# Optimization experiments

Hardware: AMD Instinct MI355X
Metric: run time of the kernel (lower is better)

Reference implementation:

```python
import jax, jax.numpy as jnp
import numpy as np

VOCAB, EMBED, HIDDEN, NCLASS = 32000, 256, 512, 2
BATCH, SEQ = 64, 512


def setup_inputs() -> dict:
    key = jax.random.key(0)
    ks = jax.random.split(key, 12)
    s_e = 1.0 / np.sqrt(HIDDEN)  # pytorch RNN init scale
    inp = {
        "x": jax.random.randint(ks[0], (BATCH, SEQ), 0, VOCAB),
        "emb": jax.random.normal(ks[1], (VOCAB, EMBED), dtype=jnp.float32),
        "W_ih0": jax.random.uniform(ks[2], (HIDDEN, EMBED), minval=-s_e, maxval=s_e),
        "W_hh0": jax.random.uniform(ks[3], (HIDDEN, HIDDEN), minval=-s_e, maxval=s_e),
        "b_ih0": jax.random.uniform(ks[4], (HIDDEN,), minval=-s_e, maxval=s_e),
        "b_hh0": jax.random.uniform(ks[5], (HIDDEN,), minval=-s_e, maxval=s_e),
        "W_ih1": jax.random.uniform(ks[6], (HIDDEN, HIDDEN), minval=-s_e, maxval=s_e),
        "W_hh1": jax.random.uniform(ks[7], (HIDDEN, HIDDEN), minval=-s_e, maxval=s_e),
        "b_ih1": jax.random.uniform(ks[8], (HIDDEN,), minval=-s_e, maxval=s_e),
        "b_hh1": jax.random.uniform(ks[9], (HIDDEN,), minval=-s_e, maxval=s_e),
        "W_out": jax.random.uniform(ks[10], (NCLASS, HIDDEN), minval=-s_e, maxval=s_e),
        "b_out": jax.random.uniform(ks[11], (NCLASS,), minval=-s_e, maxval=s_e),
    }
    return inp


def _rnn_layer(inp_bse, W_ih, W_hh, b_ih, b_hh):
    """Vanilla tanh RNN layer. inp: [B,S,E] -> out: [B,S,H]."""
    # precompute input projection for all timesteps (one big GEMM)
    xp = jnp.einsum("bse,he->bsh", inp_bse, W_ih) + b_ih + b_hh  # [B,S,H]
    B = inp_bse.shape[0]
    h0 = jnp.zeros((B, W_hh.shape[0]), dtype=inp_bse.dtype)

    def step(h, xp_t):
        h = jnp.tanh(xp_t + h @ W_hh.T)
        return h, h

    _, out = jax.lax.scan(step, h0, jnp.swapaxes(xp, 0, 1))  # out: [S,B,H]
    return jnp.swapaxes(out, 0, 1)


def reference(x, emb, W_ih0, W_hh0, b_ih0, b_hh0, W_ih1, W_hh1, b_ih1, b_hh1,
              W_out, b_out):
    h = emb[x]  # [B,S,E] embedding lookup
    h = _rnn_layer(h, W_ih0, W_hh0, b_ih0, b_hh0)  # layer 1
    h = _rnn_layer(h, W_ih1, W_hh1, b_ih1, b_hh1)  # layer 2
    pooled = jnp.mean(h, axis=1)  # avg_pool2d over (S,1) == mean over time -> [B,H]
    return pooled @ W_out.T + b_out  # [B,2]
```

## Files before the change

### kernel.cpp

```cpp
#include <hip/hip_runtime.h>
#include <math.h>

#define BB 64
#define SS 512
#define EE 256
#define HH 512

#define NGROUPS 16
#define GSLICES 8
#define LBLK 16
#define BPG 4
#define RECT 512
#define RING 64
#define BARK 32

#define SLOTF (GSLICES * 512)
#define GPKF  (2 * RING * SLOTF)


__global__ void transpose512(const float* __restrict__ in, float* __restrict__ out) {
  __shared__ float tile[32][33];
  int bx = blockIdx.x * 32, by = blockIdx.y * 32;
  int x = threadIdx.x, y0 = threadIdx.y;
  for (int dy = 0; dy < 32; dy += 8)
    tile[y0 + dy][x] = in[(size_t)(by + y0 + dy) * HH + bx + x];
  __syncthreads();
  for (int dy = 0; dy < 32; dy += 8)
    out[(size_t)(bx + y0 + dy) * HH + by + x] = tile[x][y0 + dy];
}

template <int K, bool GATHER>
__global__ __launch_bounds__(256) void xp_gemm(
    const float* __restrict__ Asrc, const int* __restrict__ xidx,
    const float* __restrict__ emb, const float* __restrict__ Wn,
    const float* __restrict__ bias1, const float* __restrict__ bias2,
    float* __restrict__ C) {
  const int tid = threadIdx.x;
  const int m0 = blockIdx.x * 64;
  const int n0 = blockIdx.y * 64;
  __shared__ alignas(16) float As[32][68];
  __shared__ alignas(16) float Bs[32][68];
  __shared__ int xs[64];
  if (GATHER) {
    if (tid < 64) xs[tid] = xidx[m0 + tid];
    __syncthreads();
  }
  float acc[4][4] = {};
  const int ty = tid >> 4, tx = tid & 15;
  const int row = tid >> 2;
  const int kc = (tid & 3) * 8;

  for (int k0 = 0; k0 < K; k0 += 32) {
    const float* ap;
    if (GATHER) ap = emb + (size_t)xs[row] * EE + (k0 + kc);
    else        ap = Asrc + (size_t)(m0 + row) * K + (k0 + kc);
    float4 av0 = *(const float4*)ap;
    float4 av1 = *(const float4*)(ap + 4);
    const float* bp = Wn + (size_t)(n0 + row) * K + (k0 + kc);
    float4 bv0 = *(const float4*)bp;
    float4 bv1 = *(const float4*)(bp + 4);
    __syncthreads();
    As[kc + 0][row] = av0.x; As[kc + 1][row] = av0.y;
    As[kc + 2][row] = av0.z; As[kc + 3][row] = av0.w;
    As[kc + 4][row] = av1.x; As[kc + 5][row] = av1.y;
    As[kc + 6][row] = av1.z; As[kc + 7][row] = av1.w;
    Bs[kc + 0][row] = bv0.x; Bs[kc + 1][row] = bv0.y;
    Bs[kc + 2][row] = bv0.z; Bs[kc + 3][row] = bv0.w;
    Bs[kc + 4][row] = bv1.x; Bs[kc + 5][row] = bv1.y;
    Bs[kc + 6][row] = bv1.z; Bs[kc + 7][row] = bv1.w;
    __syncthreads();
#pragma unroll 8
    for (int k = 0; k < 32; ++k) {
      float4 av = *(const float4*)&As[k][ty * 4];
      float4 bv = *(const float4*)&Bs[k][tx * 4];
      acc[0][0] += av.x * bv.x; acc[0][1] += av.x * bv.y;
      acc[0][2] += av.x * bv.z; acc[0][3] += av.x * bv.w;
      acc[1][0] += av.y * bv.x; acc[1][1] += av.y * bv.y;
      acc[1][2] += av.y * bv.z; acc[1][3] += av.y * bv.w;
      acc[2][0] += av.z * bv.x; acc[2][1] += av.z * bv.y;
      acc[2][2] += av.z * bv.z; acc[2][3] += av.z * bv.w;
      acc[3][0] += av.w * bv.x; acc[3][1] += av.w * bv.y;
      acc[3][2] += av.w * bv.z; acc[3][3] += av.w * bv.w;
    }
  }
  float bj[4];
#pragma unroll
  for (int j = 0; j < 4; ++j) {
    int n = n0 + tx * 4 + j;
    bj[j] = bias1[n] + bias2[n];
  }
#pragma unroll
  for (int i = 0; i < 4; ++i) {
    float4 cv = make_float4(acc[i][0] + bj[0], acc[i][1] + bj[1],
                            acc[i][2] + bj[2], acc[i][3] + bj[3]);
    *(float4*)&C[(size_t)(m0 + ty * 4 + i) * HH + n0 + tx * 4] = cv;
  }
}

__global__ void init_sync(float* __restrict__ pkts, unsigned* __restrict__ flags) {
  const size_t n = (size_t)NGROUPS * GPKF;
  const size_t stride = (size_t)gridDim.x * 256;
  for (size_t i = (size_t)blockIdx.x * 256 + threadIdx.x; i < n; i += stride)
    __hip_atomic_store(&pkts[i], 0.f, __ATOMIC_RELAXED, __HIP_MEMORY_SCOPE_SYSTEM);
  const size_t m = NGROUPS * LBLK * 32;
  for (size_t i = (size_t)blockIdx.x * 256 + threadIdx.x; i < m; i += stride)
    __hip_atomic_store(&flags[i], 0u, __ATOMIC_RELAXED, __HIP_MEMORY_SCOPE_SYSTEM);
}

__device__ __forceinline__ void fma4(float4& d, const float4 w, const float s) {
  d.x = __builtin_fmaf(w.x, s, d.x);
  d.y = __builtin_fmaf(w.y, s, d.y);
  d.z = __builtin_fmaf(w.z, s, d.z);
  d.w = __builtin_fmaf(w.w, s, d.w);
}

__device__ __forceinline__ void poll2(const float* pb, unsigned tg,
                                      float4& u0, float4& u1) {
  for (;;) {
    asm volatile(
      "global_load_dwordx4 %0, %2, off sc0 sc1\n\t"
      "global_load_dwordx4 %1, %2, off offset:16 sc0 sc1\n\t"
      "s_waitcnt vmcnt(0)"
      : "=&v"(u0), "=&v"(u1) : "v"(pb) : "memory");
    if (__float_as_uint(u0.y) == tg && __float_as_uint(u0.w) == tg &&
        __float_as_uint(u1.y) == tg && __float_as_uint(u1.w) == tg) break;
    __builtin_amdgcn_s_sleep(1);
  }
}

__device__ __forceinline__ void poll4(const float* pa, unsigned tga,
                                      const float* pb, unsigned tgb,
                                      float4& a0, float4& a1,
                                      float4& b0, float4& b1) {
  for (;;) {
    asm volatile(
      "global_load_dwordx4 %0, %4, off sc0 sc1\n\t"
      "global_load_dwordx4 %1, %4, off offset:16 sc0 sc1\n\t"
      "global_load_dwordx4 %2, %5, off sc0 sc1\n\t"
      "global_load_dwordx4 %3, %5, off offset:16 sc0 sc1\n\t"
      "s_waitcnt vmcnt(0)"
      : "=&v"(a0), "=&v"(a1), "=&v"(b0), "=&v"(b1)
      : "v"(pa), "v"(pb) : "memory");
    if (__float_as_uint(a0.y) == tga && __float_as_uint(a0.w) == tga &&
        __float_as_uint(a1.y) == tga && __float_as_uint(a1.w) == tga &&
        __float_as_uint(b0.y) == tgb && __float_as_uint(b0.w) == tgb &&
        __float_as_uint(b1.y) == tgb && __float_as_uint(b1.w) == tgb) break;
    __builtin_amdgcn_s_sleep(1);
  }
}

__device__ __forceinline__ void scat(float* hs, int q0, float4 u0, float4 u1) {
  int b = (q0 >> 6) & 3;
  int j0 = (q0 >> 8) * 64 + (q0 & 63);
  *(float4*)&hs[b * HH + j0] = make_float4(u0.x, u0.z, u1.x, u1.z);
}

__device__ __forceinline__ void fma_mv_lds(float4 acc[4], const float4 wreg[16],
                                           const float* h, int jg) {
#pragma unroll
  for (int q = 0; q < 4; ++q) {
    float4 w0 = wreg[q * 4 + 0], w1 = wreg[q * 4 + 1];
    float4 w2 = wreg[q * 4 + 2], w3 = wreg[q * 4 + 3];
#pragma unroll
    for (int b = 0; b < 4; ++b) {
      float4 hv = *(const float4*)&h[b * HH + jg * 16 + q * 4];
      fma4(acc[b], w0, hv.x);
      fma4(acc[b], w1, hv.y);
      fma4(acc[b], w2, hv.z);
      fma4(acc[b], w3, hv.w);
    }
  }
}

__global__ __launch_bounds__(RECT, 2) void rec_fused(
    const float* __restrict__ xp,
    const float* __restrict__ WThh0,
    const float* __restrict__ WTih1,
    const float* __restrict__ WThh1,
    const float* __restrict__ b_ih1,
    const float* __restrict__ b_hh1,
    float* __restrict__ pooled,
    float* __restrict__ pkts,
    unsigned* __restrict__ flags) {
  const int tid = threadIdx.x;
  const int bid = blockIdx.x;
  const int grp = bid & 15;
  const int role = bid >> 4;
  const bool isL1 = role >= GSLICES;
  const int slice = role & 7;
  const int oo4 = tid & 15;
  const int jg = tid >> 4;
  const int obase = slice * 64 + oo4 * 4;

  float4 wregA[16], wregB[16];
  {
    const float* wb = isL1 ? WThh1 : WThh0;
#pragma unroll
    for (int j = 0; j < 16; ++j)
      wregB[j] = *(const float4*)&wb[(size_t)(jg * 16 + j) * HH + obase];
#pragma unroll
    for (int j = 0; j < 16; ++j)
      asm volatile("" : "+v"(wregB[j].x), "+v"(wregB[j].y),
                        "+v"(wregB[j].z), "+v"(wregB[j].w));
  }
  if (isL1) {
#pragma unroll
    for (int j = 0; j < 16; ++j)
      wregA[j] = *(const float4*)&WTih1[(size_t)(jg * 16 + j) * HH + obase];
#pragma unroll
    for (int j = 0; j < 16; ++j)
      asm volatile("" : "+v"(wregA[j].x), "+v"(wregA[j].y),
                        "+v"(wregA[j].z), "+v"(wregA[j].w));
  }

  float* pk = pkts + (size_t)grp * GPKF;
  unsigned* flg = flags + grp * (LBLK * 32);

  __shared__ alignas(16) float hA[BPG * HH];
  __shared__ alignas(16) float hB[BPG * HH];
  __shared__ float part[2][8][16][17];

  const int wave = tid >> 6, wl = tid & 63;
  const int fo = tid & 63;
  const int fbb = (tid >> 6) & 3;
  const int fog = slice * 64 + fo;
  const size_t fxbase = (size_t)(grp * BPG + fbb) * (SS * HH) + fog;
  float pacc = 0.f;
  float bs = 0.f;
  if (tid < 256) bs = b_ih1[fog] + b_hh1[fog];

  const int q0 = tid * 4;
  const int toff = tid * 8;
  const int wpo = slice * 512 + (fbb * 64 + fo) * 2;

  for (int s = 0; s < SS; ++s) {
    const int sp = s & 1;
    float xv = 0.f;
    if (!isL1) {
      if (tid < 256) xv = xp[fxbase + (size_t)s * HH];
      if (s >= 1) {
        float4 u0, u1;
        const float* pb = pk + (size_t)((s - 1) & (RING - 1)) * SLOTF + toff;
        poll2(pb, (unsigned)s, u0, u1);
        scat(hA, q0, u0, u1);
      }
    } else {
      if (s >= 2) {
        float4 a0, a1, b0, b1;
        const float* pa = pk + (size_t)((s - 1) & (RING - 1)) * SLOTF + toff;
        const float* pb = pk + (size_t)(RING + ((s - 2) & (RING - 1))) * SLOTF + toff;
        poll4(pa, (unsigned)s, pb, (unsigned)(s - 1), a0, a1, b0, b1);
        scat(hA, q0, a0, a1);
        scat(hB, q0, b0, b1);
      } else if (s == 1) {
        float4 a0, a1;
        const float* pa = pk + (size_t)0 * SLOTF + toff;
        poll2(pa, 1u, a0, a1);
        scat(hA, q0, a0, a1);
      }
    }
    asm volatile("s_waitcnt lgkmcnt(0)" ::: "memory");
    __builtin_amdgcn_sched_barrier(0);

    float4 acc[BPG] = {{0,0,0,0},{0,0,0,0},{0,0,0,0},{0,0,0,0}};
    if (s >= 1) {
      if (!isL1) {
        fma_mv_lds(acc, wregB, hA, jg);
      } else {
        fma_mv_lds(acc, wregA, hA, jg);
        if (s >= 2) fma_mv_lds(acc, wregB, hB, jg);
      }
#pragma unroll
      for (int b = 0; b < BPG; ++b) {
        acc[b].x += __shfl_down(acc[b].x, 32); acc[b].y += __shfl_down(acc[b].y, 32);
        acc[b].z += __shfl_down(acc[b].z, 32); acc[b].w += __shfl_down(acc[b].w, 32);
        acc[b].x += __shfl_down(acc[b].x, 16); acc[b].y += __shfl_down(acc[b].y, 16);
        acc[b].z += __shfl_down(acc[b].z, 16); acc[b].w += __shfl_down(acc[b].w, 16);
      }
      if (wl < 16) {
#pragma unroll
        for (int b = 0; b < BPG; ++b) {
          part[sp][wave][wl][b * 4 + 0] = acc[b].x;
          part[sp][wave][wl][b * 4 + 1] = acc[b].y;
          part[sp][wave][wl][b * 4 + 2] = acc[b].z;
          part[sp][wave][wl][b * 4 + 3] = acc[b].w;
        }
      }
    }
    __syncthreads();

    if (tid < 256) {
      if (!isL1) {
        float v = xv;
        if (s >= 1) {
#pragma unroll
          for (int w = 0; w < 8; ++w)
            v += part[sp][w][fo >> 2][fbb * 4 + (fo & 3)];
        }
        float h = tanhf(v);
        float* pw = pk + (size_t)(s & (RING - 1)) * SLOTF + wpo;
        float2 pkt; pkt.x = h; pkt.y = __uint_as_float((unsigned)(s + 1));
        asm volatile("global_store_dwordx2 %0, %1, off sc0 sc1"
                     :: "v"(pw), "v"(pkt) : "memory");
      } else if (s >= 1) {
        float v = bs;
#pragma unroll
        for (int w = 0; w < 8; ++w)
          v += part[sp][w][fo >> 2][fbb * 4 + (fo & 3)];
        float h = tanhf(v);
        pacc += h;
        float* pw = pk + (size_t)(RING + ((s - 1) & (RING - 1))) * SLOTF + wpo;
        float2 pkt; pkt.x = h; pkt.y = __uint_as_float((unsigned)s);
        asm volatile("global_store_dwordx2 %0, %1, off sc0 sc1"
                     :: "v"(pw), "v"(pkt) : "memory");
      }
    }

    if ((s & (BARK - 1)) == (BARK - 1)) {
      unsigned bt = (unsigned)((s >> 5) + 1);
      if (tid == 0) {
        unsigned* fp = flg + role * 32;
        asm volatile("global_store_dword %0, %1, off sc0 sc1"
                     :: "v"(fp), "v"(bt) : "memory");
      }
      if (tid < LBLK) {
        const unsigned* fp = flg + tid * 32;
        unsigned v;
        do {
          asm volatile("global_load_dword %0, %1, off sc0 sc1\n\ts_waitcnt vmcnt(0)"
                       : "=v"(v) : "v"(fp) : "memory");
          if (v < bt) __builtin_amdgcn_s_sleep(2);
        } while (v < bt);
      }
      __syncthreads();
    }
  }

  if (isL1) {
    float4 a0, a1, b0, b1;
    const float* pa = pk + (size_t)((SS - 1) & (RING - 1)) * SLOTF + toff;
    const float* pb = pk + (size_t)(RING + ((SS - 2) & (RING - 1))) * SLOTF + toff;
    poll4(pa, (unsigned)SS, pb, (unsigned)(SS - 1), a0, a1, b0, b1);
    scat(hA, q0, a0, a1);
    scat(hB, q0, b0, b1);
    asm volatile("s_waitcnt lgkmcnt(0)" ::: "memory");
    __builtin_amdgcn_sched_barrier(0);
    float4 acc[BPG] = {{0,0,0,0},{0,0,0,0},{0,0,0,0},{0,0,0,0}};
    fma_mv_lds(acc, wregA, hA, jg);
    fma_mv_lds(acc, wregB, hB, jg);
#pragma unroll
    for (int b = 0; b < BPG; ++b) {
      acc[b].x += __shfl_down(acc[b].x, 32); acc[b].y += __shfl_down(acc[b].y, 32);
      acc[b].z += __shfl_down(acc[b].z, 32); acc[b].w += __shfl_down(acc[b].w, 32);
      acc[b].x += __shfl_down(acc[b].x, 16); acc[b].y += __shfl_down(acc[b].y, 16);
      acc[b].z += __shfl_down(acc[b].z, 16); acc[b].w += __shfl_down(acc[b].w, 16);
    }
    if (wl < 16) {
#pragma unroll
      for (int b = 0; b < BPG; ++b) {
        part[0][wave][wl][b * 4 + 0] = acc[b].x;
        part[0][wave][wl][b * 4 + 1] = acc[b].y;
        part[0][wave][wl][b * 4 + 2] = acc[b].z;
        part[0][wave][wl][b * 4 + 3] = acc[b].w;
      }
    }
    __syncthreads();
    if (tid < 256) {
      float v = bs;
#pragma unroll
      for (int w = 0; w < 8; ++w)
        v += part[0][w][fo >> 2][fbb * 4 + (fo & 3)];
      pacc += tanhf(v);
      pooled[(size_t)(grp * BPG + fbb) * HH + fog] = pacc * (1.0f / SS);
    }
  }
}

__global__ void out_kernel(const float* __restrict__ pooled,
                           const float* __restrict__ W_out,
                           const float* __restrict__ b_out,
                           float* __restrict__ out) {
  int tid = threadIdx.x;
  if (tid >= BB * 2) return;
  int b = tid >> 1, c = tid & 1;
  float acc = b_out[c];
  for (int k = 0; k < HH; ++k)
    acc += pooled[(size_t)b * HH + k] * W_out[(size_t)c * HH + k];
  out[(size_t)b * 2 + c] = acc;
}

extern "C" void kernel_launch(void* const* d_in, const int* in_sizes, int n_in,
                              void* d_out, int out_size, void* d_ws, size_t ws_size,
                              hipStream_t stream) {
  const int*   x     = (const int*)d_in[0];
  const float* emb   = (const float*)d_in[1];
  const float* W_ih0 = (const float*)d_in[2];
  const float* W_hh0 = (const float*)d_in[3];
  const float* b_ih0 = (const float*)d_in[4];
  const float* b_hh0 = (const float*)d_in[5];
  const float* W_ih1 = (const float*)d_in[6];
  const float* W_hh1 = (const float*)d_in[7];
  const float* b_ih1 = (const float*)d_in[8];
  const float* b_hh1 = (const float*)d_in[9];
  const float* W_out = (const float*)d_in[10];
  const float* b_out = (const float*)d_in[11];

  float* ws = (float*)d_ws;
  const size_t NBSH = (size_t)BB * SS * HH;
  const size_t PKF  = (size_t)NGROUPS * GPKF;
  float* xp      = ws;
  float* WThh0   = ws + NBSH;
  float* WTih1   = WThh0 + HH * HH;
  float* WThh1   = WTih1 + HH * HH;
  float* pooled  = WThh1 + HH * HH;
  float* pkts    = pooled + BB * HH;
  unsigned* flags = (unsigned*)(pkts + PKF);

  init_sync<<<4096, 256, 0, stream>>>(pkts, flags);

  dim3 tb(32, 8), tg(16, 16);
  transpose512<<<tg, tb, 0, stream>>>(W_hh0, WThh0);
  transpose512<<<tg, tb, 0, stream>>>(W_ih1, WTih1);
  transpose512<<<tg, tb, 0, stream>>>(W_hh1, WThh1);

  dim3 gg(512, 8);
  xp_gemm<EE, true><<<gg, 256, 0, stream>>>(nullptr, x, emb, W_ih0, b_ih0, b_hh0, xp);
  rec_fused<<<NGROUPS * LBLK, RECT, 0, stream>>>(
      xp, WThh0, WTih1, WThh1, b_ih1, b_hh1, pooled, pkts, flags);
  out_kernel<<<1, 128, 0, stream>>>(pooled, W_out, b_out, (float*)d_out);
}
```

Measured before the change: 1.833 ms.

## Split each group's batch into two half-batches pipelined through the recurrence

Each group's four batch rows are split into two halves of two rows, each with its own packet ring, LDS buffers and partial-sum buffer. Within a timestep the block computes and publishes half A, then polls and computes half B. Other blocks can start on half A while half B is still being produced, so communication latency overlaps with compute. The cost is an extra __syncthreads per step, smaller per-phase work, and more packet slots in global memory.

```diff
diff --git a/kernel.cpp b/kernel.cpp
--- a/kernel.cpp
+++ b/kernel.cpp
@@ -10,12 +10,13 @@
 #define GSLICES 8
 #define LBLK 16
 #define BPG 4
+#define BPP 2
 #define RECT 512
 #define RING 64
 #define BARK 32
 
-#define SLOTF (GSLICES * 512)
-#define GPKF  (2 * RING * SLOTF)
+#define SLOTF2 (GSLICES * 256)
+#define GPKF   (4 * RING * SLOTF2)
 
 
 __global__ void transpose512(const float* __restrict__ in, float* __restrict__ out) {
@@ -114,55 +115,39 @@
   d.w = __builtin_fmaf(w.w, s, d.w);
 }
 
-__device__ __forceinline__ void poll2(const float* pb, unsigned tg,
-                                      float4& u0, float4& u1) {
+__device__ __forceinline__ float4 poll1(const float* p, unsigned tg) {
+  float4 u;
   for (;;) {
-    asm volatile(
-      "global_load_dwordx4 %0, %2, off sc0 sc1\n\t"
-      "global_load_dwordx4 %1, %2, off offset:16 sc0 sc1\n\t"
-      "s_waitcnt vmcnt(0)"
-      : "=&v"(u0), "=&v"(u1) : "v"(pb) : "memory");
-    if (__float_as_uint(u0.y) == tg && __float_as_uint(u0.w) == tg &&
-        __float_as_uint(u1.y) == tg && __float_as_uint(u1.w) == tg) break;
+    asm volatile("global_load_dwordx4 %0, %1, off sc0 sc1\n\ts_waitcnt vmcnt(0)"
+                 : "=&v"(u) : "v"(p) : "memory");
+    if (__float_as_uint(u.y) == tg && __float_as_uint(u.w) == tg) break;
     __builtin_amdgcn_s_sleep(1);
   }
-}
-
-__device__ __forceinline__ void poll4(const float* pa, unsigned tga,
-                                      const float* pb, unsigned tgb,
-                                      float4& a0, float4& a1,
-                                      float4& b0, float4& b1) {
+  return u;
+}
+
+__device__ __forceinline__ void poll1x2(const float* pa, unsigned tga,
+                                        const float* pb, unsigned tgb,
+                                        float4& a, float4& b) {
   for (;;) {
-    asm volatile(
-      "global_load_dwordx4 %0, %4, off sc0 sc1\n\t"
-      "global_load_dwordx4 %1, %4, off offset:16 sc0 sc1\n\t"
-      "global_load_dwordx4 %2, %5, off sc0 sc1\n\t"
-      "global_load_dwordx4 %3, %5, off offset:16 sc0 sc1\n\t"
-      "s_waitcnt vmcnt(0)"
-      : "=&v"(a0), "=&v"(a1), "=&v"(b0), "=&v"(b1)
-      : "v"(pa), "v"(pb) : "memory");
-    if (__float_as_uint(a0.y) == tga && __float_as_uint(a0.w) == tga &&
-        __float_as_uint(a1.y) == tga && __float_as_uint(a1.w) == tga &&
-        __float_as_uint(b0.y) == tgb && __float_as_uint(b0.w) == tgb &&
-        __float_as_uint(b1.y) == tgb && __float_as_uint(b1.w) == tgb) break;
+    asm volatile("global_load_dwordx4 %0, %2, off sc0 sc1\n\t"
+                 "global_load_dwordx4 %1, %3, off sc0 sc1\n\t"
+                 "s_waitcnt vmcnt(0)"
+                 : "=&v"(a), "=&v"(b) : "v"(pa), "v"(pb) : "memory");
+    if (__float_as_uint(a.y) == tga && __float_as_uint(a.w) == tga &&
+        __float_as_uint(b.y) == tgb && __float_as_uint(b.w) == tgb) break;
     __builtin_amdgcn_s_sleep(1);
   }
 }
 
-__device__ __forceinline__ void scat(float* hs, int q0, float4 u0, float4 u1) {
-  int b = (q0 >> 6) & 3;
-  int j0 = (q0 >> 8) * 64 + (q0 & 63);
-  *(float4*)&hs[b * HH + j0] = make_float4(u0.x, u0.z, u1.x, u1.z);
-}
-
-__device__ __forceinline__ void fma_mv_lds(float4 acc[4], const float4 wreg[16],
-                                           const float* h, int jg) {
+__device__ __forceinline__ void fma_mv2(float4 acc[2], const float4 wreg[16],
+                                        const float* h, int jg) {
 #pragma unroll
   for (int q = 0; q < 4; ++q) {
     float4 w0 = wreg[q * 4 + 0], w1 = wreg[q * 4 + 1];
     float4 w2 = wreg[q * 4 + 2], w3 = wreg[q * 4 + 3];
 #pragma unroll
-    for (int b = 0; b < 4; ++b) {
+    for (int b = 0; b < BPP; ++b) {
       float4 hv = *(const float4*)&h[b * HH + jg * 16 + q * 4];
       fma4(acc[b], w0, hv.x);
       fma4(acc[b], w1, hv.y);
@@ -216,103 +201,166 @@
   float* pk = pkts + (size_t)grp * GPKF;
   unsigned* flg = flags + grp * (LBLK * 32);
 
-  __shared__ alignas(16) float hA[BPG * HH];
-  __shared__ alignas(16) float hB[BPG * HH];
-  __shared__ float part[2][8][16][17];
+  __shared__ alignas(16) float hs0A[BPP * HH];
+  __shared__ alignas(16) float hs0B[BPP * HH];
+  __shared__ alignas(16) float hs1A[BPP * HH];
+  __shared__ alignas(16) float hs1B[BPP * HH];
+  __shared__ float part[2][8][16][9];
 
   const int wave = tid >> 6, wl = tid & 63;
   const int fo = tid & 63;
   const int fbb = (tid >> 6) & 3;
+  const int fbl = (tid >> 6) & 1;
   const int fog = slice * 64 + fo;
   const size_t fxbase = (size_t)(grp * BPG + fbb) * (SS * HH) + fog;
   float pacc = 0.f;
   float bs = 0.f;
   if (tid < 256) bs = b_ih1[fog] + b_hh1[fog];
 
-  const int q0 = tid * 4;
-  const int toff = tid * 8;
-  const int wpo = slice * 512 + (fbb * 64 + fo) * 2;
+  const int toff = wave * 256 + wl * 4;
+  const int wpo = slice * 256 + fo * 4 + fbl * 2;
 
   for (int s = 0; s < SS; ++s) {
-    const int sp = s & 1;
     float xv = 0.f;
-    if (!isL1) {
-      if (tid < 256) xv = xp[fxbase + (size_t)s * HH];
-      if (s >= 1) {
-        float4 u0, u1;
-        const float* pb = pk + (size_t)((s - 1) & (RING - 1)) * SLOTF + toff;
-        poll2(pb, (unsigned)s, u0, u1);
-        scat(hA, q0, u0, u1);
-      }
-    } else {
-      if (s >= 2) {
-        float4 a0, a1, b0, b1;
-        const float* pa = pk + (size_t)((s - 1) & (RING - 1)) * SLOTF + toff;
-        const float* pb = pk + (size_t)(RING + ((s - 2) & (RING - 1))) * SLOTF + toff;
-        poll4(pa, (unsigned)s, pb, (unsigned)(s - 1), a0, a1, b0, b1);
-        scat(hA, q0, a0, a1);
-        scat(hB, q0, b0, b1);
-      } else if (s == 1) {
-        float4 a0, a1;
-        const float* pa = pk + (size_t)0 * SLOTF + toff;
-        poll2(pa, 1u, a0, a1);
-        scat(hA, q0, a0, a1);
+    if (!isL1 && tid < 256) xv = xp[fxbase + (size_t)s * HH];
+
+    if (s >= 1) {
+      const float* p0 = pk + (size_t)((0 * RING) + ((s - 1) & (RING - 1))) * SLOTF2 + toff;
+      if (!isL1) {
+        float4 u = poll1(p0, (unsigned)s);
+        hs0A[tid] = u.x; hs0A[HH + tid] = u.z;
+      } else if (s >= 2) {
+        const float* p1 = pk + (size_t)((2 * RING) + ((s - 2) & (RING - 1))) * SLOTF2 + toff;
+        float4 a, b;
+        poll1x2(p0, (unsigned)s, p1, (unsigned)(s - 1), a, b);
+        hs0A[tid] = a.x; hs0A[HH + tid] = a.z;
+        hs1A[tid] = b.x; hs1A[HH + tid] = b.z;
+      } else {
+        float4 a = poll1(p0, 1u);
+        hs0A[tid] = a.x; hs0A[HH + tid] = a.z;
       }
     }
     asm volatile("s_waitcnt lgkmcnt(0)" ::: "memory");
     __builtin_amdgcn_sched_barrier(0);
-
-    float4 acc[BPG] = {{0,0,0,0},{0,0,0,0},{0,0,0,0},{0,0,0,0}};
-    if (s >= 1) {
-      if (!isL1) {
-        fma_mv_lds(acc, wregB, hA, jg);
-      } else {
-        fma_mv_lds(acc, wregA, hA, jg);
-        if (s >= 2) fma_mv_lds(acc, wregB, hB, jg);
-      }
-#pragma unroll
-      for (int b = 0; b < BPG; ++b) {
-        acc[b].x += __shfl_down(acc[b].x, 32); acc[b].y += __shfl_down(acc[b].y, 32);
-        acc[b].z += __shfl_down(acc[b].z, 32); acc[b].w += __shfl_down(acc[b].w, 32);
-        acc[b].x += __shfl_down(acc[b].x, 16); acc[b].y += __shfl_down(acc[b].y, 16);
-        acc[b].z += __shfl_down(acc[b].z, 16); acc[b].w += __shfl_down(acc[b].w, 16);
-      }
-      if (wl < 16) {
-#pragma unroll
-        for (int b = 0; b < BPG; ++b) {
-          part[sp][wave][wl][b * 4 + 0] = acc[b].x;
-          part[sp][wave][wl][b * 4 + 1] = acc[b].y;
-          part[sp][wave][wl][b * 4 + 2] = acc[b].z;
-          part[sp][wave][wl][b * 4 + 3] = acc[b].w;
-        }
-      }
-    }
-    __syncthreads();
-
-    if (tid < 256) {
+    {
+      float4 acc[BPP] = {{0,0,0,0},{0,0,0,0}};
+      if (s >= 1) {
+        if (!isL1) fma_mv2(acc, wregB, hs0A, jg);
+        else {
+          fma_mv2(acc, wregA, hs0A, jg);
+          if (s >= 2) fma_mv2(acc, wregB, hs1A, jg);
+        }
+#pragma unroll
+        for (int b = 0; b < BPP; ++b) {
+          acc[b].x += __shfl_down(acc[b].x, 32); acc[b].y += __shfl_down(acc[b].y, 32);
+          acc[b].z += __shfl_down(acc[b].z, 32); acc[b].w += __shfl_down(acc[b].w, 32);
+          acc[b].x += __shfl_down(acc[b].x, 16); acc[b].y += __shfl_down(acc[b].y, 16);
+          acc[b].z += __shfl_down(acc[b].z, 16); acc[b].w += __shfl_down(acc[b].w, 16);
+        }
+        if (wl < 16) {
+#pragma unroll
+          for (int b = 0; b < BPP; ++b) {
+            part[0][wave][wl][b * 4 + 0] = acc[b].x;
+            part[0][wave][wl][b * 4 + 1] = acc[b].y;
+            part[0][wave][wl][b * 4 + 2] = acc[b].z;
+            part[0][wave][wl][b * 4 + 3] = acc[b].w;
+          }
+        }
+      }
+    }
+    __syncthreads();
+    if (tid < 128) {
       if (!isL1) {
         float v = xv;
         if (s >= 1) {
 #pragma unroll
-          for (int w = 0; w < 8; ++w)
-            v += part[sp][w][fo >> 2][fbb * 4 + (fo & 3)];
+          for (int w = 0; w < 8; ++w) v += part[0][w][fo >> 2][fbl * 4 + (fo & 3)];
         }
         float h = tanhf(v);
-        float* pw = pk + (size_t)(s & (RING - 1)) * SLOTF + wpo;
-        float2 pkt; pkt.x = h; pkt.y = __uint_as_float((unsigned)(s + 1));
+        float* pw = pk + (size_t)((0 * RING) + (s & (RING - 1))) * SLOTF2 + wpo;
+        float2 pp; pp.x = h; pp.y = __uint_as_float((unsigned)(s + 1));
         asm volatile("global_store_dwordx2 %0, %1, off sc0 sc1"
-                     :: "v"(pw), "v"(pkt) : "memory");
+                     :: "v"(pw), "v"(pp) : "memory");
       } else if (s >= 1) {
         float v = bs;
 #pragma unroll
-        for (int w = 0; w < 8; ++w)
-          v += part[sp][w][fo >> 2][fbb * 4 + (fo & 3)];
+        for (int w = 0; w < 8; ++w) v += part[0][w][fo >> 2][fbl * 4 + (fo & 3)];
         float h = tanhf(v);
         pacc += h;
-        float* pw = pk + (size_t)(RING + ((s - 1) & (RING - 1))) * SLOTF + wpo;
-        float2 pkt; pkt.x = h; pkt.y = __uint_as_float((unsigned)s);
+        float* pw = pk + (size_t)((2 * RING) + ((s - 1) & (RING - 1))) * SLOTF2 + wpo;
+        float2 pp; pp.x = h; pp.y = __uint_as_float((unsigned)s);
         asm volatile("global_store_dwordx2 %0, %1, off sc0 sc1"
-                     :: "v"(pw), "v"(pkt) : "memory");
+                     :: "v"(pw), "v"(pp) : "memory");
+      }
+    }
+
+    if (s >= 1) {
+      const float* p0 = pk + (size_t)((1 * RING) + ((s - 1) & (RING - 1))) * SLOTF2 + toff;
+      if (!isL1) {
+        float4 u = poll1(p0, (unsigned)s);
+        hs0B[tid] = u.x; hs0B[HH + tid] = u.z;
+      } else if (s >= 2) {
+        const float* p1 = pk + (size_t)((3 * RING) + ((s - 2) & (RING - 1))) * SLOTF2 + toff;
+        float4 a, b;
+        poll1x2(p0, (unsigned)s, p1, (unsigned)(s - 1), a, b);
+        hs0B[tid] = a.x; hs0B[HH + tid] = a.z;
+        hs1B[tid] = b.x; hs1B[HH + tid] = b.z;
+      } else {
+        float4 a = poll1(p0, 1u);
+        hs0B[tid] = a.x; hs0B[HH + tid] = a.z;
+      }
+    }
+    asm volatile("s_waitcnt lgkmcnt(0)" ::: "memory");
+    __builtin_amdgcn_sched_barrier(0);
+    {
+      float4 acc[BPP] = {{0,0,0,0},{0,0,0,0}};
+      if (s >= 1) {
+        if (!isL1) fma_mv2(acc, wregB, hs0B, jg);
+        else {
+          fma_mv2(acc, wregA, hs0B, jg);
+          if (s >= 2) fma_mv2(acc, wregB, hs1B, jg);
+        }
+#pragma unroll
+        for (int b = 0; b < BPP; ++b) {
+          acc[b].x += __shfl_down(acc[b].x, 32); acc[b].y += __shfl_down(acc[b].y, 32);
+          acc[b].z += __shfl_down(acc[b].z, 32); acc[b].w += __shfl_down(acc[b].w, 32);
+          acc[b].x += __shfl_down(acc[b].x, 16); acc[b].y += __shfl_down(acc[b].y, 16);
+          acc[b].z += __shfl_down(acc[b].z, 16); acc[b].w += __shfl_down(acc[b].w, 16);
+        }
+        if (wl < 16) {
+#pragma unroll
+          for (int b = 0; b < BPP; ++b) {
+            part[1][wave][wl][b * 4 + 0] = acc[b].x;
+            part[1][wave][wl][b * 4 + 1] = acc[b].y;
+            part[1][wave][wl][b * 4 + 2] = acc[b].z;
+            part[1][wave][wl][b * 4 + 3] = acc[b].w;
+          }
+        }
+      }
+    }
+    __syncthreads();
+    if (tid >= 128 && tid < 256) {
+      if (!isL1) {
+        float v = xv;
+        if (s >= 1) {
+#pragma unroll
+          for (int w = 0; w < 8; ++w) v += part[1][w][fo >> 2][fbl * 4 + (fo & 3)];
+        }
+        float h = tanhf(v);
+        float* pw = pk + (size_t)((1 * RING) + (s & (RING - 1))) * SLOTF2 + wpo;
+        float2 pp; pp.x = h; pp.y = __uint_as_float((unsigned)(s + 1));
+        asm volatile("global_store_dwordx2 %0, %1, off sc0 sc1"
+                     :: "v"(pw), "v"(pp) : "memory");
+      } else if (s >= 1) {
+        float v = bs;
+#pragma unroll
+        for (int w = 0; w < 8; ++w) v += part[1][w][fo >> 2][fbl * 4 + (fo & 3)];
+        float h = tanhf(v);
+        pacc += h;
+        float* pw = pk + (size_t)((3 * RING) + ((s - 1) & (RING - 1))) * SLOTF2 + wpo;
+        float2 pp; pp.x = h; pp.y = __uint_as_float((unsigned)s);
+        asm volatile("global_store_dwordx2 %0, %1, off sc0 sc1"
+                     :: "v"(pw), "v"(pp) : "memory");
       }
     }
 
@@ -337,39 +385,51 @@
   }
 
   if (isL1) {
-    float4 a0, a1, b0, b1;
-    const float* pa = pk + (size_t)((SS - 1) & (RING - 1)) * SLOTF + toff;
-    const float* pb = pk + (size_t)(RING + ((SS - 2) & (RING - 1))) * SLOTF + toff;
-    poll4(pa, (unsigned)SS, pb, (unsigned)(SS - 1), a0, a1, b0, b1);
-    scat(hA, q0, a0, a1);
-    scat(hB, q0, b0, b1);
+    {
+      const float* p0 = pk + (size_t)((0 * RING) + ((SS - 1) & (RING - 1))) * SLOTF2 + toff;
+      const float* p1 = pk + (size_t)((2 * RING) + ((SS - 2) & (RING - 1))) * SLOTF2 + toff;
+      float4 a, b;
+      poll1x2(p0, (unsigned)SS, p1, (unsigned)(SS - 1), a, b);
+      hs0A[tid] = a.x; hs0A[HH + tid] = a.z;
+      hs1A[tid] = b.x; hs1A[HH + tid] = b.z;
+      const float* q0 = pk + (size_t)((1 * RING) + ((SS - 1) & (RING - 1))) * SLOTF2 + toff;
+      const float* q1 = pk + (size_t)((3 * RING) + ((SS - 2) & (RING - 1))) * SLOTF2 + toff;
+      float4 c, d;
+      poll1x2(q0, (unsigned)SS, q1, (unsigned)(SS - 1), c, d);
+      hs0B[tid] = c.x; hs0B[HH + tid] = c.z;
+      hs1B[tid] = d.x; hs1B[HH + tid] = d.z;
+    }
     asm volatile("s_waitcnt lgkmcnt(0)" ::: "memory");
     __builtin_amdgcn_sched_barrier(0);
-    float4 acc[BPG] = {{0,0,0,0},{0,0,0,0},{0,0,0,0},{0,0,0,0}};
-    fma_mv_lds(acc, wregA, hA, jg);
-    fma_mv_lds(acc, wregB, hB, jg);
-#pragma unroll
-    for (int b = 0; b < BPG; ++b) {
-      acc[b].x += __shfl_down(acc[b].x, 32); acc[b].y += __shfl_down(acc[b].y, 32);
-      acc[b].z += __shfl_down(acc[b].z, 32); acc[b].w += __shfl_down(acc[b].w, 32);
-      acc[b].x += __shfl_down(acc[b].x, 16); acc[b].y += __shfl_down(acc[b].y, 16);
-      acc[b].z += __shfl_down(acc[b].z, 16); acc[b].w += __shfl_down(acc[b].w, 16);
-    }
-    if (wl < 16) {
-#pragma unroll
-      for (int b = 0; b < BPG; ++b) {
-        part[0][wave][wl][b * 4 + 0] = acc[b].x;
-        part[0][wave][wl][b * 4 + 1] = acc[b].y;
-        part[0][wave][wl][b * 4 + 2] = acc[b].z;
-        part[0][wave][wl][b * 4 + 3] = acc[b].w;
+    for (int ph = 0; ph < 2; ++ph) {
+      float4 acc[BPP] = {{0,0,0,0},{0,0,0,0}};
+      const float* h0 = ph ? hs0B : hs0A;
+      const float* h1 = ph ? hs1B : hs1A;
+      fma_mv2(acc, wregA, h0, jg);
+      fma_mv2(acc, wregB, h1, jg);
+#pragma unroll
+      for (int b = 0; b < BPP; ++b) {
+        acc[b].x += __shfl_down(acc[b].x, 32); acc[b].y += __shfl_down(acc[b].y, 32);
+        acc[b].z += __shfl_down(acc[b].z, 32); acc[b].w += __shfl_down(acc[b].w, 32);
+        acc[b].x += __shfl_down(acc[b].x, 16); acc[b].y += __shfl_down(acc[b].y, 16);
+        acc[b].z += __shfl_down(acc[b].z, 16); acc[b].w += __shfl_down(acc[b].w, 16);
+      }
+      if (wl < 16) {
+#pragma unroll
+        for (int b = 0; b < BPP; ++b) {
+          part[ph][wave][wl][b * 4 + 0] = acc[b].x;
+          part[ph][wave][wl][b * 4 + 1] = acc[b].y;
+          part[ph][wave][wl][b * 4 + 2] = acc[b].z;
+          part[ph][wave][wl][b * 4 + 3] = acc[b].w;
+        }
       }
     }
     __syncthreads();
     if (tid < 256) {
+      int ph = tid >> 7;
       float v = bs;
 #pragma unroll
-      for (int w = 0; w < 8; ++w)
-        v += part[0][w][fo >> 2][fbb * 4 + (fo & 3)];
+      for (int w = 0; w < 8; ++w) v += part[ph][w][fo >> 2][fbl * 4 + (fo & 3)];
       pacc += tanhf(v);
       pooled[(size_t)(grp * BPG + fbb) * HH + fog] = pacc * (1.0f / SS);
     }
```

Measured after the change: 1.677 ms (median of 2 runs). -8.5%, faster.
